# Optimization experiments

Measured on AMD Instinct MI355X. Metric: run time of the kernel, lower is better.

## Reference

```python
import jax, jax.numpy as jnp
import numpy as np

B, H, S = 16, 1024, 2048

def setup_inputs() -> dict:
    key = jax.random.key(0)
    kf, kz, ki = jax.random.split(key, 3)
    f = jax.random.uniform(kf, (B, H, S), dtype=jnp.float32)
    z = jax.random.normal(kz, (B, H, S), dtype=jnp.float32)
    i = jax.random.uniform(ki, (B, H, S), dtype=jnp.float32)
    return {"f": f, "z": z, "i": i}

def reference(f, z, i):
    # Inputs are [batch, hidden, seq]; recurrence runs over seq:
    #   h_t = f_t * h_{t-1} + i_t * z_t, h_{-1} = 0
    fs = jnp.transpose(f, (2, 0, 1))  # [S, B, H]
    xs = jnp.transpose(i * z, (2, 0, 1))  # [S, B, H]

    def step(h_prev, fx):
        f_t, x_t = fx
        h_t = f_t * h_prev + x_t
        return h_t, h_t

    h0 = jnp.zeros(fs.shape[1:], dtype=fs.dtype)
    _, hs = jax.lax.scan(step, h0, (fs, xs))  # [S, B, H]
    return jnp.transpose(hs, (1, 2, 0))  # [B, H, S]
```

## Files before the change

### kernel.cpp

```cpp
#include <hip/hip_runtime.h>


constexpr int S_LEN  = 2048;
constexpr int WAVES  = 4;
constexpr int TPB    = 64 * WAVES;
constexpr int K_SUB  = S_LEN / 256;

__global__ __launch_bounds__(TPB) void ifo_scan_kernel(
    const float* __restrict__ f,
    const float* __restrict__ z,
    const float* __restrict__ iin,
    float* __restrict__ out,
    int n_rows)
{
    const int lane = threadIdx.x & 63;
    const int wv   = threadIdx.x >> 6;
    const size_t row = (size_t)blockIdx.x * WAVES + wv;
    if (row >= (size_t)n_rows) return;
    const size_t base = row * S_LEN;

    const float4* __restrict__ F = reinterpret_cast<const float4*>(f   + base);
    const float4* __restrict__ Z = reinterpret_cast<const float4*>(z   + base);
    const float4* __restrict__ I = reinterpret_cast<const float4*>(iin + base);
    float4* __restrict__ O = reinterpret_cast<float4*>(out + base);

    float4 ff[K_SUB], xx[K_SUB];
    #pragma unroll
    for (int k = 0; k < K_SUB; ++k) {
        ff[k] = F[k * 64 + lane];
        const float4 zz = Z[k * 64 + lane];
        const float4 ii = I[k * 64 + lane];
        xx[k].x = ii.x * zz.x;
        xx[k].y = ii.y * zz.y;
        xx[k].z = ii.z * zz.z;
        xx[k].w = ii.w * zz.w;
    }

    float a[K_SUB], b[K_SUB];
    #pragma unroll
    for (int k = 0; k < K_SUB; ++k) {
        float A = ff[k].x, B = xx[k].x;
        A = ff[k].y * A;  B = ff[k].y * B + xx[k].y;
        A = ff[k].z * A;  B = ff[k].z * B + xx[k].z;
        A = ff[k].w * A;  B = ff[k].w * B + xx[k].w;
        a[k] = A; b[k] = B;
    }

    #pragma unroll
    for (int k = 0; k < K_SUB; ++k) {
        #pragma unroll
        for (int d = 1; d < 64; d <<= 1) {
            float a_up = __shfl_up(a[k], d);
            float b_up = __shfl_up(b[k], d);
            if (lane >= d) {
                b[k] = a[k] * b_up + b[k];
                a[k] = a[k] * a_up;
            }
        }
    }

    float h_carry = 0.0f;
    #pragma unroll
    for (int k = 0; k < K_SUB; ++k) {
        float ea = __shfl_up(a[k], 1);
        float eb = __shfl_up(b[k], 1);
        if (lane == 0) { ea = 1.0f; eb = 0.0f; }
        float h = ea * h_carry + eb;

        const float ta = __shfl(a[k], 63);
        const float tb = __shfl(b[k], 63);
        const float next = ta * h_carry + tb;

        float4 oo;
        h = ff[k].x * h + xx[k].x;  oo.x = h;
        h = ff[k].y * h + xx[k].y;  oo.y = h;
        h = ff[k].z * h + xx[k].z;  oo.z = h;
        h = ff[k].w * h + xx[k].w;  oo.w = h;
        O[k * 64 + lane] = oo;

        h_carry = next;
    }
}

extern "C" void kernel_launch(void* const* d_in, const int* in_sizes, int n_in,
                              void* d_out, int out_size, void* d_ws, size_t ws_size,
                              hipStream_t stream) {
    const float* f = (const float*)d_in[0];
    const float* z = (const float*)d_in[1];
    const float* i = (const float*)d_in[2];
    float* out = (float*)d_out;

    const int rows = out_size / S_LEN;
    const int grid = (rows + WAVES - 1) / WAVES;
    ifo_scan_kernel<<<grid, TPB, 0, stream>>>(f, z, i, out, rows);
}
```

Baseline: 390.6 us.

## Stream chunks with prefetch depth and fuse scan phases per chunk

Replaces the load-all-then-scan structure with a per-chunk loop that prefetches three chunks ahead, fusing the local reduction, wave scan, carry application and store for each chunk. The carry is now applied by shuffling the combined prefix value instead of separate shuffles of a and b, and outputs are computed in parallel form from the per-lane prefixes. Stores become nontemporal. The aim is to overlap memory loads with the scan arithmetic and cut register pressure, at the cost of a serial carry dependency across chunks and some loss of load batching.

After: 397.4 us. Within noise of the previous version (+1.7%).

```diff
diff --git a/kernel.cpp b/kernel.cpp
--- a/kernel.cpp
+++ b/kernel.cpp
@@ -1,10 +1,13 @@
 #include <hip/hip_runtime.h>
 
+
+typedef float f32x4 __attribute__((ext_vector_type(4)));
 
 constexpr int S_LEN  = 2048;
 constexpr int WAVES  = 4;
 constexpr int TPB    = 64 * WAVES;
 constexpr int K_SUB  = S_LEN / 256;
+constexpr int PRE    = 3;
 
 __global__ __launch_bounds__(TPB) void ifo_scan_kernel(
     const float* __restrict__ f,
@@ -22,63 +25,60 @@
     const float4* __restrict__ F = reinterpret_cast<const float4*>(f   + base);
     const float4* __restrict__ Z = reinterpret_cast<const float4*>(z   + base);
     const float4* __restrict__ I = reinterpret_cast<const float4*>(iin + base);
-    float4* __restrict__ O = reinterpret_cast<float4*>(out + base);
+    f32x4* __restrict__ O = reinterpret_cast<f32x4*>(out + base);
 
-    float4 ff[K_SUB], xx[K_SUB];
+    float4 fq[K_SUB], zq[K_SUB], iq[K_SUB];
     #pragma unroll
-    for (int k = 0; k < K_SUB; ++k) {
-        ff[k] = F[k * 64 + lane];
-        const float4 zz = Z[k * 64 + lane];
-        const float4 ii = I[k * 64 + lane];
-        xx[k].x = ii.x * zz.x;
-        xx[k].y = ii.y * zz.y;
-        xx[k].z = ii.z * zz.z;
-        xx[k].w = ii.w * zz.w;
+    for (int k = 0; k < PRE; ++k) {
+        fq[k] = F[k * 64 + lane];
+        zq[k] = Z[k * 64 + lane];
+        iq[k] = I[k * 64 + lane];
     }
 
-    float a[K_SUB], b[K_SUB];
-    #pragma unroll
-    for (int k = 0; k < K_SUB; ++k) {
-        float A = ff[k].x, B = xx[k].x;
-        A = ff[k].y * A;  B = ff[k].y * B + xx[k].y;
-        A = ff[k].z * A;  B = ff[k].z * B + xx[k].z;
-        A = ff[k].w * A;  B = ff[k].w * B + xx[k].w;
-        a[k] = A; b[k] = B;
-    }
+    float carry = 0.0f;
 
     #pragma unroll
     for (int k = 0; k < K_SUB; ++k) {
+        if (k + PRE < K_SUB) {
+            fq[k + PRE] = F[(k + PRE) * 64 + lane];
+            zq[k + PRE] = Z[(k + PRE) * 64 + lane];
+            iq[k + PRE] = I[(k + PRE) * 64 + lane];
+        }
+
+        const float4 ffv = fq[k], zzv = zq[k], iiv = iq[k];
+        const float x0 = iiv.x * zzv.x;
+        const float x1 = iiv.y * zzv.y;
+        const float x2 = iiv.z * zzv.z;
+        const float x3 = iiv.w * zzv.w;
+
+        const float A0 = ffv.x;      const float B0 = x0;
+        const float A1 = ffv.y * A0; const float B1 = ffv.y * B0 + x1;
+        const float A2 = ffv.z * A1; const float B2 = ffv.z * B1 + x2;
+        const float A3 = ffv.w * A2; const float B3 = ffv.w * B2 + x3;
+
+        float sa = A3, sb = B3;
         #pragma unroll
         for (int d = 1; d < 64; d <<= 1) {
-            float a_up = __shfl_up(a[k], d);
-            float b_up = __shfl_up(b[k], d);
+            const float a_up = __shfl_up(sa, d);
+            const float b_up = __shfl_up(sb, d);
             if (lane >= d) {
-                b[k] = a[k] * b_up + b[k];
-                a[k] = a[k] * a_up;
+                sb = sa * b_up + sb;
+                sa = sa * a_up;
             }
         }
-    }
 
-    float h_carry = 0.0f;
-    #pragma unroll
-    for (int k = 0; k < K_SUB; ++k) {
-        float ea = __shfl_up(a[k], 1);
-        float eb = __shfl_up(b[k], 1);
-        if (lane == 0) { ea = 1.0f; eb = 0.0f; }
-        float h = ea * h_carry + eb;
+        const float v = sa * carry + sb;
+        float hin = __shfl_up(v, 1);
+        if (lane == 0) hin = carry;
 
-        const float ta = __shfl(a[k], 63);
-        const float tb = __shfl(b[k], 63);
-        const float next = ta * h_carry + tb;
+        f32x4 o;
+        o.x = A0 * hin + B0;
+        o.y = A1 * hin + B1;
+        o.z = A2 * hin + B2;
+        o.w = A3 * hin + B3;
+        __builtin_nontemporal_store(o, O + k * 64 + lane);
 
-        float4 oo;
-        h = ff[k].x * h + xx[k].x;  oo.x = h;
-        h = ff[k].y * h + xx[k].y;  oo.y = h;
-        h = ff[k].z * h + xx[k].z;  oo.z = h;
-        h = ff[k].w * h + xx[k].w;  oo.w = h;
-        O[k * 64 + lane] = oo;
-
-        h_carry = next;
+        carry = __shfl(v, 63);
     }
 }
 
```
